# Kernel tuning notes

Measured on AMD Instinct MI355X. Metric: run time of the kernel, lower is better.

Reference implementation:

```python
import jax, jax.numpy as jnp
import numpy as np

EPS = 1e-8  # torch CosineSimilarity default eps
MARGIN = 0.1


def _normalize(x):
    # row-normalize with eps clamp on the norm (matches torch cosine_similarity)
    n = jnp.sqrt(jnp.sum(x * x, axis=-1, keepdims=True))
    return x / jnp.maximum(n, EPS)


def setup_inputs() -> dict:
    key = jax.random.key(0)
    k1, k2, k3 = jax.random.split(key, 3)
    B, D, C = 1024, 512, 100000
    inputs = jax.random.normal(k1, (B, D), dtype=jnp.float32)
    class_embeddings = jax.random.normal(k2, (C, D), dtype=jnp.float32)
    targets = jax.random.randint(k3, (B,), 0, C, dtype=jnp.int64)
    return {"inputs": inputs, "class_embeddings": class_embeddings, "targets": targets}


def reference(inputs, class_embeddings, targets):
    B = inputs.shape[0]
    x_n = _normalize(inputs)                    # [B, D]
    c_n = _normalize(class_embeddings)          # [C, D]
    # cosine similarity against ALL classes: the repeat/expand in the original
    # is just this normalized matmul.
    scores = jnp.einsum('bd,cd->bc', x_n, c_n)  # [B, C]
    # cosine similarity with the target class embedding
    target_cos = scores[jnp.arange(B), targets]  # [B]
    hinge = jnp.maximum(0.0, MARGIN - target_cos[:, None] + scores)  # [B, C]
    per_sample = jnp.sum(hinge, axis=1) - MARGIN  # subtract the target's own margin term
    return jnp.mean(per_sample)
```

## Files before the change

kernel.cpp:

```cpp
#include <hip/hip_runtime.h>
#include <stdint.h>

#define NB 1024
#define ND 512
#define NC 100000
#define MT 782
#define MARGINF 0.1f

using bf16x8 = __attribute__((ext_vector_type(8))) short;
using f32x4  = __attribute__((ext_vector_type(4))) float;

__device__ __forceinline__ uint32_t f2bf(float f) {
  uint32_t u = __float_as_uint(f);
  return (u + 0x7fffu + ((u >> 16) & 1u)) >> 16;
}
__device__ __forceinline__ uint32_t pack2bf(float x, float y) {
  return f2bf(x) | (f2bf(y) << 16);
}

__global__ __launch_bounds__(256)
void normalize_relayout(const float* __restrict__ src, uint16_t* __restrict__ dst) {
  __shared__ uint16_t lds[16][520];
  const int lane = threadIdx.x & 63;
  const int wv = threadIdx.x >> 6;
  const size_t R0 = (size_t)blockIdx.x << 4;
  #pragma unroll
  for (int i = 0; i < 4; ++i) {
    const int r = (wv << 2) + i;
    const float4* s = (const float4*)(src + (R0 + r) * ND) + (lane << 1);
    float4 a = s[0], b = s[1];
    float ss = a.x*a.x + a.y*a.y + a.z*a.z + a.w*a.w
             + b.x*b.x + b.y*b.y + b.z*b.z + b.w*b.w;
    #pragma unroll
    for (int o = 32; o; o >>= 1) ss += __shfl_xor(ss, o);
    const float inv = 1.0f / fmaxf(sqrtf(ss), 1e-8f);
    uint4 o4;
    o4.x = pack2bf(a.x * inv, a.y * inv);
    o4.y = pack2bf(a.z * inv, a.w * inv);
    o4.z = pack2bf(b.x * inv, b.y * inv);
    o4.w = pack2bf(b.z * inv, b.w * inv);
    *(uint4*)(&lds[r][lane << 3]) = o4;
  }
  __syncthreads();
  uint16_t* out = dst + ((size_t)blockIdx.x << 13);
  #pragma unroll
  for (int c = 0; c < 4; ++c) {
    const int idx = (c << 8) + threadIdx.x;
    const int kc = idx >> 6, g = (idx >> 4) & 3, rs = idx & 15;
    uint4 v = *(const uint4*)(&lds[rs][(kc << 5) + (g << 3)]);
    ((uint4*)out)[idx] = v;
  }
}

__global__ void target_cos_kernel(const float* __restrict__ x,
                                  const float* __restrict__ cls,
                                  const int* __restrict__ tgt,
                                  float* __restrict__ t) {
  const int b = blockIdx.x;
  const int row = tgt[b];
  const float2* xr = (const float2*)(x + (size_t)b * ND);
  const float2* cr = (const float2*)(cls + (size_t)row * ND);
  float2 xv = xr[threadIdx.x], cv = cr[threadIdx.x];
  float sx = xv.x * xv.x + xv.y * xv.y;
  float sc = cv.x * cv.x + cv.y * cv.y;
  float sd = xv.x * cv.x + xv.y * cv.y;
  #pragma unroll
  for (int o = 32; o; o >>= 1) {
    sx += __shfl_down(sx, o);
    sc += __shfl_down(sc, o);
    sd += __shfl_down(sd, o);
  }
  __shared__ float r[3][4];
  const int wv = threadIdx.x >> 6;
  if ((threadIdx.x & 63) == 0) { r[0][wv] = sx; r[1][wv] = sc; r[2][wv] = sd; }
  __syncthreads();
  if (threadIdx.x == 0) {
    float ax = r[0][0] + r[0][1] + r[0][2] + r[0][3];
    float ac = r[1][0] + r[1][1] + r[1][2] + r[1][3];
    float ad = r[2][0] + r[2][1] + r[2][2] + r[2][3];
    t[b] = ad / (fmaxf(sqrtf(ax), 1e-8f) * fmaxf(sqrtf(ac), 1e-8f));
  }
}

__global__ __launch_bounds__(256, 3)
void hinge_gemm_frag(const uint16_t* __restrict__ Wf,
                     const uint16_t* __restrict__ Xf,
                     const float* __restrict__ t,
                     float* __restrict__ accum) {
  const int id = blockIdx.x;
  const int nt = (id >> 3) & 7;
  const int mt = (id & 7) + ((id >> 6) << 3);
  if (mt >= MT) return;
  const int m0 = mt << 7, n0 = nt << 7;
  const int lane = threadIdx.x & 63;
  const int wv = threadIdx.x >> 6;
  const int wm = wv & 1, wn = wv >> 1;
  const int lr = lane & 15;

  const uint16_t* pA[4];
  const uint16_t* pB[4];
  #pragma unroll
  for (int ms = 0; ms < 4; ++ms) {
    const int fA = (m0 >> 4) + (wm << 2) + ms;
    pA[ms] = Wf + (size_t)fA * 8192 + (lane << 3);
  }
  #pragma unroll
  for (int j = 0; j < 4; ++j) {
    const int fB = (n0 >> 4) + (wn << 2) + j;
    pB[j] = Xf + (size_t)fB * 8192 + (lane << 3);
  }

  f32x4 acc[4][4];
  #pragma unroll
  for (int i = 0; i < 4; ++i)
    #pragma unroll
    for (int j = 0; j < 4; ++j)
      acc[i][j] = (f32x4){0.f, 0.f, 0.f, 0.f};

  bf16x8 ab[2][4], bb[2][4];
  #pragma unroll
  for (int ms = 0; ms < 4; ++ms) ab[0][ms] = *(const bf16x8*)(pA[ms]);
  #pragma unroll
  for (int j = 0; j < 4; ++j)    bb[0][j]  = *(const bf16x8*)(pB[j]);

  #pragma unroll
  for (int kk = 0; kk < 16; ++kk) {
    const int cur = kk & 1, nxt = cur ^ 1;
    if (kk < 15) {
      #pragma unroll
      for (int ms = 0; ms < 4; ++ms)
        ab[nxt][ms] = *(const bf16x8*)(pA[ms] + ((kk + 1) << 9));
      #pragma unroll
      for (int j = 0; j < 4; ++j)
        bb[nxt][j] = *(const bf16x8*)(pB[j] + ((kk + 1) << 9));
    }
    #pragma unroll
    for (int ms = 0; ms < 4; ++ms)
      #pragma unroll
      for (int j = 0; j < 4; ++j)
        acc[ms][j] = __builtin_amdgcn_mfma_f32_16x16x32_bf16(ab[cur][ms], bb[cur][j], acc[ms][j], 0, 0, 0);
  }

  float local = 0.f;
  const int rb4 = (lane >> 4) << 2;
  #pragma unroll
  for (int j = 0; j < 4; ++j) {
    const int n = n0 + (wn << 6) + (j << 4) + lr;
    const float base = MARGINF - t[n];
    #pragma unroll
    for (int ms = 0; ms < 4; ++ms) {
      const int mr = m0 + (wm << 6) + (ms << 4) + rb4;
      f32x4 v = acc[ms][j];
      #pragma unroll
      for (int rr = 0; rr < 4; ++rr)
        if (mr + rr < NC) local += fmaxf(base + v[rr], 0.f);
    }
  }
  #pragma unroll
  for (int o = 32; o; o >>= 1) local += __shfl_down(local, o);
  __shared__ float part[4];
  if (lane == 0) part[wv] = local;
  __syncthreads();
  if (threadIdx.x == 0)
    atomicAdd(&accum[id & 63], part[0] + part[1] + part[2] + part[3]);
}

__global__ void finalize_kernel(const float* __restrict__ accum, float* __restrict__ out) {
  float s = 0.f;
  #pragma unroll
  for (int i = 0; i < 64; ++i) s += accum[i];
  out[0] = s * (1.0f / (float)NB) - MARGINF;
}

#define WS_WF 0
#define WS_XF 102400000ull
#define WS_T  103448576ull
#define WS_ACC 103452672ull

extern "C" void kernel_launch(void* const* d_in, const int* in_sizes, int n_in,
                              void* d_out, int out_size, void* d_ws, size_t ws_size,
                              hipStream_t stream) {
  const float* inputs = (const float*)d_in[0];
  const float* cls    = (const float*)d_in[1];
  const int*   tgt    = (const int*)d_in[2];
  float* out = (float*)d_out;
  char* ws = (char*)d_ws;
  uint16_t* Wf = (uint16_t*)(ws + WS_WF);
  uint16_t* Xf = (uint16_t*)(ws + WS_XF);
  float* t     = (float*)(ws + WS_T);
  float* accum = (float*)(ws + WS_ACC);

  (void)hipMemsetAsync(accum, 0, 64 * sizeof(float), stream);
  normalize_relayout<<<64, 256, 0, stream>>>(inputs, Xf);
  normalize_relayout<<<6250, 256, 0, stream>>>(cls, Wf);
  target_cos_kernel<<<NB, 256, 0, stream>>>(inputs, cls, tgt, t);
  hinge_gemm_frag<<<6272, 256, 0, stream>>>(Wf, Xf, t, accum);
  finalize_kernel<<<1, 1, 0, stream>>>(accum, out);
}
```

Measured before the change: 449.1 us.

## Stage GEMM tiles through LDS with async global_load_lds four-deep pipeline

Replaces the register-only fragment GEMM with a 256x256-tile, 512-thread kernel. It streams A and B fragments into a 4-buffer LDS ring via global_load_lds, with explicit vmcnt waits and barriers. MFMA priority is raised while computing. The larger tiles are meant to cut redundant global reads of the class embeddings and overlap loads with compute. The cost is 128KB of LDS per block, which limits occupancy and adds extra barriers.

Result: faster. 426.9 us (-4.9%).

```diff
diff --git a/kernel.cpp b/kernel.cpp
--- a/kernel.cpp
+++ b/kernel.cpp
@@ -4,7 +4,7 @@
 #define NB 1024
 #define ND 512
 #define NC 100000
-#define MT 782
+#define MTILES 391
 #define MARGINF 0.1f
 
 using bf16x8 = __attribute__((ext_vector_type(8))) short;
@@ -82,74 +82,111 @@
   }
 }
 
-__global__ __launch_bounds__(256, 3)
-void hinge_gemm_frag(const uint16_t* __restrict__ Wf,
+__device__ __forceinline__ void gload16(const char* g, char* l) {
+  __builtin_amdgcn_global_load_lds(
+      (__attribute__((address_space(1))) void*)(g),
+      (__attribute__((address_space(3))) void*)(l), 16, 0, 0);
+}
+#define WAITVM(N)  asm volatile("s_waitcnt vmcnt(" #N ")" ::: "memory")
+#define LGKM0()    asm volatile("s_waitcnt lgkmcnt(0)" ::: "memory")
+#define MEMFENCE() asm volatile("" ::: "memory")
+
+__global__ __launch_bounds__(512, 2)
+void hinge_gemm_pipe(const uint16_t* __restrict__ Wf,
                      const uint16_t* __restrict__ Xf,
                      const float* __restrict__ t,
                      float* __restrict__ accum) {
   const int id = blockIdx.x;
-  const int nt = (id >> 3) & 7;
-  const int mt = (id & 7) + ((id >> 6) << 3);
-  if (mt >= MT) return;
-  const int m0 = mt << 7, n0 = nt << 7;
+  const int mt = (id & 7) + ((id >> 5) << 3);
+  const int nt = (id >> 3) & 3;
+  if (mt >= MTILES) return;
+
+  __shared__ __align__(1024) char lds[131072];
+  __shared__ float part[8];
+
   const int lane = threadIdx.x & 63;
   const int wv = threadIdx.x >> 6;
-  const int wm = wv & 1, wn = wv >> 1;
-  const int lr = lane & 15;
-
-  const uint16_t* pA[4];
-  const uint16_t* pB[4];
-  #pragma unroll
-  for (int ms = 0; ms < 4; ++ms) {
-    const int fA = (m0 >> 4) + (wm << 2) + ms;
-    pA[ms] = Wf + (size_t)fA * 8192 + (lane << 3);
-  }
-  #pragma unroll
-  for (int j = 0; j < 4; ++j) {
-    const int fB = (n0 >> 4) + (wn << 2) + j;
-    pB[j] = Xf + (size_t)fB * 8192 + (lane << 3);
-  }
-
-  f32x4 acc[4][4];
-  #pragma unroll
-  for (int i = 0; i < 4; ++i)
+  const int wm = wv & 1;
+  const int wn = wv >> 1;
+  const int laneoff = lane << 4;
+  const int aoff = wm << 13;
+  const int boff = (1 << 14) + (wn << 12);
+
+  const char* gsrc[4];
+  int dsto[4];
+  #pragma unroll
+  for (int i = 0; i < 4; ++i) {
+    const int sl = (wv << 2) + i;
+    if (sl < 16) {
+      gsrc[i] = (const char*)Wf + (((size_t)(mt * 16 + sl)) << 14) + laneoff;
+      dsto[i] = sl << 10;
+    } else {
+      gsrc[i] = (const char*)Xf + (((size_t)(nt * 16 + (sl - 16))) << 14) + laneoff;
+      dsto[i] = (1 << 14) + ((sl - 16) << 10);
+    }
+  }
+
+  f32x4 acc[8][4];
+  #pragma unroll
+  for (int i = 0; i < 8; ++i)
     #pragma unroll
     for (int j = 0; j < 4; ++j)
       acc[i][j] = (f32x4){0.f, 0.f, 0.f, 0.f};
 
-  bf16x8 ab[2][4], bb[2][4];
-  #pragma unroll
-  for (int ms = 0; ms < 4; ++ms) ab[0][ms] = *(const bf16x8*)(pA[ms]);
-  #pragma unroll
-  for (int j = 0; j < 4; ++j)    bb[0][j]  = *(const bf16x8*)(pB[j]);
-
-  #pragma unroll
-  for (int kk = 0; kk < 16; ++kk) {
-    const int cur = kk & 1, nxt = cur ^ 1;
-    if (kk < 15) {
-      #pragma unroll
-      for (int ms = 0; ms < 4; ++ms)
-        ab[nxt][ms] = *(const bf16x8*)(pA[ms] + ((kk + 1) << 9));
-      #pragma unroll
-      for (int j = 0; j < 4; ++j)
-        bb[nxt][j] = *(const bf16x8*)(pB[j] + ((kk + 1) << 9));
-    }
-    #pragma unroll
-    for (int ms = 0; ms < 4; ++ms)
-      #pragma unroll
-      for (int j = 0; j < 4; ++j)
-        acc[ms][j] = __builtin_amdgcn_mfma_f32_16x16x32_bf16(ab[cur][ms], bb[cur][j], acc[ms][j], 0, 0, 0);
-  }
-
+#define STAGE(T) {                                                         \
+    char* lb_ = lds + (((T) & 3) << 15);                                   \
+    _Pragma("unroll")                                                      \
+    for (int i_ = 0; i_ < 4; ++i_)                                         \
+      gload16(gsrc[i_] + ((size_t)(T) << 10), lb_ + dsto[i_]);             \
+  }
+
+#define COMPUTE(KT) {                                                      \
+    const char* base_ = lds + (((KT) & 3) << 15);                          \
+    bf16x8 a_[8]; bf16x8 b_[4];                                            \
+    _Pragma("unroll")                                                      \
+    for (int ms_ = 0; ms_ < 8; ++ms_)                                      \
+      a_[ms_] = *(const bf16x8*)(base_ + aoff + (ms_ << 10) + laneoff);    \
+    _Pragma("unroll")                                                      \
+    for (int j_ = 0; j_ < 4; ++j_)                                         \
+      b_[j_] = *(const bf16x8*)(base_ + boff + (j_ << 10) + laneoff);      \
+    LGKM0();                                                               \
+    __builtin_amdgcn_sched_barrier(0);                                     \
+    __builtin_amdgcn_s_barrier();   \
+    __builtin_amdgcn_s_setprio(1);                                         \
+    _Pragma("unroll")                                                      \
+    for (int ms_ = 0; ms_ < 8; ++ms_)                                      \
+      _Pragma("unroll")                                                    \
+      for (int j_ = 0; j_ < 4; ++j_)                                       \
+        acc[ms_][j_] = __builtin_amdgcn_mfma_f32_16x16x32_bf16(            \
+            a_[ms_], b_[j_], acc[ms_][j_], 0, 0, 0);                       \
+    __builtin_amdgcn_s_setprio(0);                                         \
+  }
+
+  STAGE(0); STAGE(1); STAGE(2);
+
+  #pragma unroll 1
+  for (int kt = 0; kt < 13; ++kt) {
+    STAGE(kt + 3);
+    WAITVM(12);
+    __builtin_amdgcn_s_barrier();
+    MEMFENCE();
+    COMPUTE(kt);
+  }
+  WAITVM(8);  __builtin_amdgcn_s_barrier(); MEMFENCE(); COMPUTE(13);
+  WAITVM(4);  __builtin_amdgcn_s_barrier(); MEMFENCE(); COMPUTE(14);
+  WAITVM(0);  __builtin_amdgcn_s_barrier(); MEMFENCE(); COMPUTE(15);
+
+  const int m0 = mt << 8, n0 = nt << 8;
+  const int lr = lane & 15;
+  const int rb4 = (lane >> 4) << 2;
   float local = 0.f;
-  const int rb4 = (lane >> 4) << 2;
   #pragma unroll
   for (int j = 0; j < 4; ++j) {
     const int n = n0 + (wn << 6) + (j << 4) + lr;
     const float base = MARGINF - t[n];
     #pragma unroll
-    for (int ms = 0; ms < 4; ++ms) {
-      const int mr = m0 + (wm << 6) + (ms << 4) + rb4;
+    for (int ms = 0; ms < 8; ++ms) {
+      const int mr = m0 + (wm << 7) + (ms << 4) + rb4;
       f32x4 v = acc[ms][j];
       #pragma unroll
       for (int rr = 0; rr < 4; ++rr)
@@ -158,11 +195,16 @@
   }
   #pragma unroll
   for (int o = 32; o; o >>= 1) local += __shfl_down(local, o);
-  __shared__ float part[4];
   if (lane == 0) part[wv] = local;
   __syncthreads();
-  if (threadIdx.x == 0)
-    atomicAdd(&accum[id & 63], part[0] + part[1] + part[2] + part[3]);
+  if (threadIdx.x == 0) {
+    float s = 0.f;
+    #pragma unroll
+    for (int i = 0; i < 8; ++i) s += part[i];
+    atomicAdd(&accum[id & 63], s);
+  }
+#undef STAGE
+#undef COMPUTE
 }
 
 __global__ void finalize_kernel(const float* __restrict__ accum, float* __restrict__ out) {
@@ -194,6 +236,6 @@
   normalize_relayout<<<64, 256, 0, stream>>>(inputs, Xf);
   normalize_relayout<<<6250, 256, 0, stream>>>(cls, Wf);
   target_cos_kernel<<<NB, 256, 0, stream>>>(inputs, cls, tgt, t);
-  hinge_gemm_frag<<<6272, 256, 0, stream>>>(Wf, Xf, t, accum);
+  hinge_gemm_pipe<<<1568, 512, 0, stream>>>(Wf, Xf, t, accum);
   finalize_kernel<<<1, 1, 0, stream>>>(accum, out);
 }
```
